# Kernel optimization log

Hardware: AMD Instinct MI355X
Metric: run time of the kernel (lower is better)

## Reference

```python
import jax, jax.numpy as jnp
import numpy as np

B, N_COLS, N_PROMPTS, D = 1024, 256, 128, 256


def _ln(x, g, b, eps=1e-5):
    m = jnp.mean(x, axis=-1, keepdims=True)
    v = jnp.mean(jnp.square(x - m), axis=-1, keepdims=True)
    return (x - m) * jax.lax.rsqrt(v + eps) * g + b


def setup_inputs() -> dict:
    key = jax.random.key(0)
    ks = jax.random.split(key, 10)
    d_rs = D ** -0.5
    return {
        "x": jax.random.normal(ks[0], (B, N_COLS), jnp.float32),
        "prev_cell_out": jax.random.normal(ks[1], (B, N_PROMPTS, D), jnp.float32),
        "feature_emb_weight": jax.random.uniform(ks[2], (N_COLS, D), jnp.float32, -d_rs, d_rs),
        "feature_emb_bias": jax.random.uniform(ks[3], (N_COLS, D), jnp.float32, -d_rs, d_rs),
        "ln_emb_g": jnp.ones((D,), jnp.float32),
        "ln_emb_b": jnp.zeros((D,), jnp.float32),
        "ln_col_g": jnp.ones((D,), jnp.float32),
        "ln_col_b": jnp.zeros((D,), jnp.float32),
        "ln_prompt_g": jnp.ones((D,), jnp.float32),
        "ln_prompt_b": jnp.zeros((D,), jnp.float32),
        # torch Linear(2*D, D): weight [D, 2*D], y = x @ W^T + b
        "dense_imp_w": jax.random.normal(ks[4], (D, 2 * D), jnp.float32) * (2 * D) ** -0.5,
        "dense_imp_b": jnp.zeros((D,), jnp.float32),
        "emb_column": jax.random.normal(ks[5], (N_COLS, D), jnp.float32) * 0.01,
        "emb_prompt": jax.random.normal(ks[6], (N_PROMPTS, D), jnp.float32) * 0.01,
        # dense_expand = Linear(1, n_prompts): weight [n_prompts,1] squeezed -> [n_prompts]
        "expand_w": jax.random.normal(ks[7], (N_PROMPTS,), jnp.float32),
        "expand_b": jax.random.normal(ks[8], (N_PROMPTS,), jnp.float32) * 0.01,
    }


def reference(x, prev_cell_out, feature_emb_weight, feature_emb_bias,
              ln_emb_g, ln_emb_b, ln_col_g, ln_col_b, ln_prompt_g, ln_prompt_b,
              dense_imp_w, dense_imp_b, emb_column, emb_prompt,
              expand_w, expand_b):
    # feature embedding: [B, N, D]
    x_emb = jax.nn.relu(jnp.einsum('bn,nd->bnd', x, feature_emb_weight) + feature_emb_bias)
    x_emb = _ln(x_emb, ln_emb_g, ln_emb_b)
    # prompt update with residual
    xp = jnp.broadcast_to(emb_prompt[None], (x.shape[0], N_PROMPTS, D))  # [B, P, D]
    cat = jnp.concatenate([_ln(xp, ln_prompt_g, ln_prompt_b), prev_cell_out], axis=-1)  # [B, P, 2D]
    xp = jnp.einsum('bpk,dk->bpd', cat, dense_imp_w) + dense_imp_b + xp
    # column keys (shared across batch)
    col = _ln(emb_column, ln_col_g, ln_col_b)  # [N, D]
    mask = jax.nn.softmax(jnp.einsum('bpd,nd->bpn', xp, col), axis=-1)  # [B, P, N]
    V = jnp.einsum('bpn,bnd->bpd', mask, x_emb)  # [B, P, D]
    return V * (1.0 + expand_w)[None, :, None] + expand_b[None, :, None]
```

## Files before the change

kernel.cpp:

```cpp
#include <hip/hip_runtime.h>

#define NCOLS 256
#define NP    128
#define DD    256

typedef _Float16 half2 __attribute__((ext_vector_type(2)));
typedef _Float16 half4 __attribute__((ext_vector_type(4)));
typedef float    f32x4 __attribute__((ext_vector_type(4)));

#define MFMA16(a,b,c) __builtin_amdgcn_mfma_f32_16x16x16f16(a,b,c,0,0,0)

#define WS_COL_LN   0
#define WS_LNP      262144
#define WS_BASE     393216
#define WS_BLOG     524288
#define WS_CW16     655360
#define WS_WB16     786432

#define LDS_CW0   3072
#define LDS_XE0   35840
#define LDS_CW1   68608
#define LDS_XE1   101376
#define SMEM_MAIN 134144


__global__ __launch_bounds__(256) void k0a(
    const float* __restrict__ emb_column, const float* __restrict__ emb_prompt,
    const float* __restrict__ ln_col_g, const float* __restrict__ ln_col_b,
    const float* __restrict__ ln_prompt_g, const float* __restrict__ ln_prompt_b,
    const float* __restrict__ few, const float* __restrict__ feb,
    char* __restrict__ ws)
{
    __shared__ float red[10];
    int blk = blockIdx.x, tid = threadIdx.x;
    if (blk < 384) {
        const float *src, *g, *bb; float* dst;
        if (blk < 256) { int r = blk;     src = emb_column + r*DD; g = ln_col_g;    bb = ln_col_b;    dst = (float*)(ws + WS_COL_LN) + r*DD; }
        else           { int r = blk-256; src = emb_prompt + r*DD; g = ln_prompt_g; bb = ln_prompt_b; dst = (float*)(ws + WS_LNP) + r*DD; }
        float v = src[tid];
        float s = v, q = v*v;
        #pragma unroll
        for (int off = 32; off; off >>= 1) { s += __shfl_xor(s, off); q += __shfl_xor(q, off); }
        int wid = tid >> 6, lane = tid & 63;
        if (lane == 0) { red[wid] = s; red[4+wid] = q; }
        __syncthreads();
        if (tid == 0) {
            float S = red[0]+red[1]+red[2]+red[3];
            float Q = red[4]+red[5]+red[6]+red[7];
            float mu = S * (1.0f/DD);
            float var = Q * (1.0f/DD) - mu*mu;
            red[8] = mu; red[9] = rsqrtf(var + 1e-5f);
        }
        __syncthreads();
        dst[tid] = (v - red[8]) * red[9] * g[tid] + bb[tid];
    } else {
        int base = (blk - 384) * 512;
        half2* wb = (half2*)(ws + WS_WB16);
        #pragma unroll
        for (int j = 0; j < 2; ++j) {
            int idx = base + j*256 + tid;
            half2 h; h[0] = (_Float16)few[idx]; h[1] = (_Float16)feb[idx];
            wb[idx] = h;
        }
    }
}

__global__ __launch_bounds__(256) void k0b(
    const float* __restrict__ diw, const float* __restrict__ dib,
    const float* __restrict__ emb_prompt, char* __restrict__ ws)
{
    __shared__ float rowv[DD];
    int blk = blockIdx.x, tid = threadIdx.x;
    if (blk < 256) {
        int n = blk;
        const float* col_ln = (const float*)(ws + WS_COL_LN);
        rowv[tid] = col_ln[n*DD + tid];
        __syncthreads();
        float acc = 0.f;
        #pragma unroll 4
        for (int d = 0; d < DD; ++d) acc += rowv[d] * diw[d*512 + 256 + tid];
        int nt = n >> 4, lr = n & 15;
        int kc = tid >> 4, lq = (tid >> 2) & 3, j = tid & 3;
        ((_Float16*)(ws + WS_CW16))[((kc*16 + nt)*64 + lq*16 + lr)*4 + j] = (_Float16)acc;
    } else {
        int p = blk - 256;
        const float* lnp = (const float*)(ws + WS_LNP);
        rowv[tid] = lnp[p*DD + tid];
        __syncthreads();
        float acc = 0.f;
        #pragma unroll 4
        for (int k = 0; k < DD; ++k) acc += rowv[k] * diw[tid*512 + k];
        ((float*)(ws + WS_BASE))[p*DD + tid] = acc + dib[tid] + emb_prompt[p*DD + tid];
    }
}

__global__ __launch_bounds__(256) void k0c(char* __restrict__ ws)
{
    __shared__ float bs[DD];
    int p = blockIdx.x, n = threadIdx.x;
    const float* base   = (const float*)(ws + WS_BASE);
    const float* col_ln = (const float*)(ws + WS_COL_LN);
    bs[n] = base[p*DD + n];
    __syncthreads();
    float acc = 0.f;
    #pragma unroll 4
    for (int d = 0; d < DD; ++d) acc += bs[d] * col_ln[n*DD + d];
    ((float*)(ws + WS_BLOG))[p*DD + n] = acc;
}

__global__ __launch_bounds__(512, 2) void trompt_main(
    const float* __restrict__ x, const float* __restrict__ prev,
    const float* __restrict__ expand_w, const float* __restrict__ expand_b,
    const float* __restrict__ ln_emb_g, const float* __restrict__ ln_emb_b,
    const char* __restrict__ ws, float* __restrict__ out)
{
    extern __shared__ char smem[];
    float* x_s  = (float*)(smem);
    float* g_s  = (float*)(smem + 1024);
    float* bb_s = (float*)(smem + 2048);

    const char*  cwbase = ws + WS_CW16;
    const half2* WB     = (const half2*)(ws + WS_WB16);

    int b = blockIdx.x;
    int tid = threadIdx.x;
    int w = tid >> 6, l = tid & 63, lq = l >> 4, lr = l & 15;
    int p = 16*w + lr;

    if (tid < 256) {
        x_s[tid]  = x[b*NCOLS + tid];
        g_s[tid]  = ln_emb_g[tid];
        bb_s[tid] = ln_emb_b[tid];
    }

    half4 pfrag[16];
    {
        const float* prow = prev + ((size_t)b*NP + p)*DD + 4*lq;
        #pragma unroll
        for (int kc = 0; kc < 16; ++kc) {
            f32x4 v = *(const f32x4*)(prow + 16*kc);
            half4 h;
            #pragma unroll
            for (int j = 0; j < 4; ++j) h[j] = (_Float16)v[j];
            pfrag[kc] = h;
        }
    }

    auto stage_cw = [&](int c, char* dstbuf) {
        #pragma unroll
        for (int i = 0; i < 4; ++i) {
            int u = tid + 512*i;
            int kc = u >> 7, rem = u & 127;
            uint4 v = *(const uint4*)(cwbase + kc*8192 + c*2048 + rem*16);
            *(uint4*)(dstbuf + u*16) = v;
        }
    };

    auto compute_xe = [&](int c, char* xebuf) {
        #pragma unroll
        for (int gi = 0; gi < 2; ++gi) {
            int g = w + 8*gi;
            int kc2 = g >> 2, lq2 = g & 3;
            float vj[4][4];
            #pragma unroll
            for (int j = 0; j < 4; ++j) {
                int n = c*64 + 16*kc2 + 4*lq2 + j;
                float xv = x_s[n];
                const half2* wbrow = WB + n*DD;
                float s = 0.f, q = 0.f;
                #pragma unroll
                for (int cc = 0; cc < 4; ++cc) {
                    half2 pp = wbrow[l + 64*cc];
                    float e = fmaf(xv, (float)pp[0], (float)pp[1]);
                    e = e > 0.f ? e : 0.f;
                    vj[j][cc] = e; s += e; q += e*e;
                }
                #pragma unroll
                for (int off = 32; off; off >>= 1) { s += __shfl_xor(s, off); q += __shfl_xor(q, off); }
                float mu = s * (1.0f/DD);
                float rs = rsqrtf(q*(1.0f/DD) - mu*mu + 1e-5f);
                #pragma unroll
                for (int cc = 0; cc < 4; ++cc) {
                    int d = l + 64*cc;
                    vj[j][cc] = (vj[j][cc]-mu)*rs*g_s[d] + bb_s[d];
                }
            }
            #pragma unroll
            for (int cc = 0; cc < 4; ++cc) {
                int dt = 4*cc + (l >> 4);
                half4 h;
                #pragma unroll
                for (int j = 0; j < 4; ++j) h[j] = (_Float16)vj[j][cc];
                *(half4*)(xebuf + (((kc2*16 + dt)*64) + lq2*16 + lr)*8) = h;
            }
        }
    };

    stage_cw(0, smem + LDS_CW0);
    __syncthreads();
    compute_xe(0, smem + LDS_XE0);

    f32x4 acc_v[16];
    #pragma unroll
    for (int dt = 0; dt < 16; ++dt) acc_v[dt] = (f32x4){0.f,0.f,0.f,0.f};
    float m = -1e30f, ll = 0.f;

    const float* blrow = (const float*)(ws + WS_BLOG) + (size_t)p*DD + 4*lq;

    __syncthreads();

    for (int c = 0; c < 4; ++c) {
        char* cwc = smem + ((c & 1) ? LDS_CW1 : LDS_CW0);
        char* xec = smem + ((c & 1) ? LDS_XE1 : LDS_XE0);
        char* cwn = smem + ((c & 1) ? LDS_CW0 : LDS_CW1);
        char* xen = smem + ((c & 1) ? LDS_XE0 : LDS_XE1);

        uint4 st[4];
        if (c < 3) {
            #pragma unroll
            for (int i = 0; i < 4; ++i) {
                int u = tid + 512*i;
                int kc = u >> 7, rem = u & 127;
                st[i] = *(const uint4*)(cwbase + kc*8192 + (c+1)*2048 + rem*16);
            }
        }

        f32x4 acc_c[4];
        #pragma unroll
        for (int nt = 0; nt < 4; ++nt) acc_c[nt] = *(const f32x4*)(blrow + 64*c + 16*nt);
        const char* cwl = cwc + l*8;
        #pragma unroll
        for (int kc = 0; kc < 16; ++kc) {
            const char* fb = cwl + kc*2048;
            half4 a0 = *(const half4*)(fb);
            half4 a1 = *(const half4*)(fb + 512);
            half4 a2 = *(const half4*)(fb + 1024);
            half4 a3 = *(const half4*)(fb + 1536);
            half4 bp = pfrag[kc];
            acc_c[0] = MFMA16(a0, bp, acc_c[0]);
            acc_c[1] = MFMA16(a1, bp, acc_c[1]);
            acc_c[2] = MFMA16(a2, bp, acc_c[2]);
            acc_c[3] = MFMA16(a3, bp, acc_c[3]);
        }

        float pmax = -1e30f;
        #pragma unroll
        for (int nt = 0; nt < 4; ++nt)
            #pragma unroll
            for (int r = 0; r < 4; ++r) pmax = fmaxf(pmax, acc_c[nt][r]);
        pmax = fmaxf(pmax, __shfl_xor(pmax, 16));
        pmax = fmaxf(pmax, __shfl_xor(pmax, 32));
        float mnew = fmaxf(m, pmax);
        float f = __expf(m - mnew);
        m = mnew;
        ll *= f;
        #pragma unroll
        for (int dt = 0; dt < 16; ++dt)
            #pragma unroll
            for (int r = 0; r < 4; ++r) acc_v[dt][r] *= f;

        float csum = 0.f;
        half4 p16c[4];
        #pragma unroll
        for (int nt = 0; nt < 4; ++nt) {
            half4 h;
            #pragma unroll
            for (int r = 0; r < 4; ++r) {
                float e = __expf(acc_c[nt][r] - m);
                csum += e;
                h[r] = (_Float16)e;
            }
            p16c[nt] = h;
        }
        csum += __shfl_xor(csum, 16);
        csum += __shfl_xor(csum, 32);
        ll += csum;

        if (c < 3) {
            compute_xe(c+1, xen);
            #pragma unroll
            for (int i = 0; i < 4; ++i) {
                int u = tid + 512*i;
                *(uint4*)(cwn + u*16) = st[i];
            }
        }

        const char* xel = xec + l*8;
        #pragma unroll
        for (int kc2 = 0; kc2 < 4; ++kc2) {
            half4 bp = p16c[kc2];
            const char* xb = xel + kc2*8192;
            #pragma unroll
            for (int dt = 0; dt < 16; ++dt) {
                half4 a = *(const half4*)(xb + dt*512);
                acc_v[dt] = MFMA16(a, bp, acc_v[dt]);
            }
        }

        __syncthreads();
    }

    {
        float sw = (1.0f + expand_w[p]) / ll;
        float sb = expand_b[p];
        float* orow = out + ((size_t)b*NP + p)*DD + 4*lq;
        #pragma unroll
        for (int dt = 0; dt < 16; ++dt) {
            f32x4 v = acc_v[dt];
            #pragma unroll
            for (int r = 0; r < 4; ++r) v[r] = v[r]*sw + sb;
            *(f32x4*)(orow + 16*dt) = v;
        }
    }
}

extern "C" void kernel_launch(void* const* d_in, const int* in_sizes, int n_in,
                              void* d_out, int out_size, void* d_ws, size_t ws_size,
                              hipStream_t stream) {
    (void)in_sizes; (void)n_in; (void)out_size; (void)ws_size;
    const float* x           = (const float*)d_in[0];
    const float* prev        = (const float*)d_in[1];
    const float* few         = (const float*)d_in[2];
    const float* feb         = (const float*)d_in[3];
    const float* ln_emb_g    = (const float*)d_in[4];
    const float* ln_emb_b    = (const float*)d_in[5];
    const float* ln_col_g    = (const float*)d_in[6];
    const float* ln_col_b    = (const float*)d_in[7];
    const float* ln_prompt_g = (const float*)d_in[8];
    const float* ln_prompt_b = (const float*)d_in[9];
    const float* diw         = (const float*)d_in[10];
    const float* dib         = (const float*)d_in[11];
    const float* emb_column  = (const float*)d_in[12];
    const float* emb_prompt  = (const float*)d_in[13];
    const float* expand_w    = (const float*)d_in[14];
    const float* expand_b    = (const float*)d_in[15];
    char* ws = (char*)d_ws;
    float* out = (float*)d_out;

    k0a<<<512, 256, 0, stream>>>(emb_column, emb_prompt, ln_col_g, ln_col_b,
                                 ln_prompt_g, ln_prompt_b, few, feb, ws);
    k0b<<<384, 256, 0, stream>>>(diw, dib, emb_prompt, ws);
    k0c<<<128, 256, 0, stream>>>(ws);

    (void)hipFuncSetAttribute(reinterpret_cast<const void*>(trompt_main),
                              hipFuncAttributeMaxDynamicSharedMemorySize, SMEM_MAIN);
    trompt_main<<<1024, 512, SMEM_MAIN, stream>>>(x, prev, expand_w, expand_b,
                                                  ln_emb_g, ln_emb_b, ws, out);
}
```

Before: 202.0 us.

## Split fused attention kernel into logit-softmax and PV kernels with fp16 P buffer

Replaces the single flash-style kernel, which used online softmax, with two kernels. The first computes logits and a full softmax per half of the prompts and writes normalized fp16 probabilities into the output buffer as scratch. The second recomputes the embedding tiles and accumulates P·X_emb, then overwrites the output in place. The aim is lower LDS and register pressure per kernel, for higher occupancy and no online rescaling. The cost is an extra global round trip for P and a second launch.

After: 218.9 us. +8.3%, slower.

```diff
diff --git a/kernel.cpp b/kernel.cpp
--- a/kernel.cpp
+++ b/kernel.cpp
@@ -17,11 +17,8 @@
 #define WS_CW16     655360
 #define WS_WB16     786432
 
-#define LDS_CW0   3072
-#define LDS_XE0   35840
-#define LDS_CW1   68608
-#define LDS_XE1   101376
-#define SMEM_MAIN 134144
+#define SMEM_LOGIT 67584
+#define SMEM_PV    34816
 
 
 __global__ __launch_bounds__(256) void k0a(
@@ -108,186 +105,212 @@
     ((float*)(ws + WS_BLOG))[p*DD + n] = acc;
 }
 
-__global__ __launch_bounds__(512, 2) void trompt_main(
-    const float* __restrict__ x, const float* __restrict__ prev,
+__global__ __launch_bounds__(512, 4) void k_logit(
+    const float* __restrict__ prev, const char* __restrict__ ws,
+    char* __restrict__ pbuf)
+{
+    extern __shared__ char smem[];
+    float* sm_m = (float*)(smem + 65536);
+    float* sm_l = (float*)(smem + 66560);
+
+    const char* cwbase = ws + WS_CW16;
+
+    int bid = blockIdx.x;
+    int b = bid >> 1, ph = bid & 1;
+    int tid = threadIdx.x;
+    int w = tid >> 6, l = tid & 63, lq = l >> 4, lr = l & 15;
+    int pt = w >> 1, nh = w & 1;
+    int pl = 16*pt + lr;
+    int p  = 64*ph + pl;
+
+    half4 pfrag[16];
+    {
+        const float* prow = prev + ((size_t)b*NP + p)*DD + 4*lq;
+        #pragma unroll
+        for (int kc = 0; kc < 16; ++kc) {
+            f32x4 v = *(const f32x4*)(prow + 16*kc);
+            half4 h;
+            #pragma unroll
+            for (int j = 0; j < 4; ++j) h[j] = (_Float16)v[j];
+            pfrag[kc] = h;
+        }
+    }
+
+    auto stage_cw = [&](int c, char* dst) {
+        #pragma unroll
+        for (int i = 0; i < 4; ++i) {
+            int u = tid + 512*i;
+            int kc = u >> 7, ntg = (u >> 5) & 3, rem = u & 31;
+            uint4 v = *(const uint4*)(cwbase + kc*8192 + c*2048 + ntg*512 + rem*16);
+            *(uint4*)(dst + u*16) = v;
+        }
+    };
+
+    f32x4 acc[8];
+    {
+        const float* blrow = (const float*)(ws + WS_BLOG) + (size_t)p*DD + 4*lq;
+        #pragma unroll
+        for (int a = 0; a < 8; ++a)
+            acc[a] = *(const f32x4*)(blrow + 16*(4*(a>>1) + 2*nh + (a&1)));
+    }
+
+    stage_cw(0, smem);
+    __syncthreads();
+
+    #pragma unroll
+    for (int c = 0; c < 4; ++c) {
+        char* cwc = smem + ((c & 1) ? 32768 : 0);
+        char* cwn = smem + ((c & 1) ? 0 : 32768);
+
+        uint4 st[4];
+        if (c < 3) {
+            #pragma unroll
+            for (int i = 0; i < 4; ++i) {
+                int u = tid + 512*i;
+                int kc = u >> 7, ntg = (u >> 5) & 3, rem = u & 31;
+                st[i] = *(const uint4*)(cwbase + kc*8192 + (c+1)*2048 + ntg*512 + rem*16);
+            }
+        }
+
+        const char* cwl = cwc + l*8 + nh*1024;
+        #pragma unroll
+        for (int kc = 0; kc < 16; ++kc) {
+            const char* fb = cwl + kc*2048;
+            half4 a0 = *(const half4*)(fb);
+            half4 a1 = *(const half4*)(fb + 512);
+            half4 bp = pfrag[kc];
+            acc[2*c]   = MFMA16(a0, bp, acc[2*c]);
+            acc[2*c+1] = MFMA16(a1, bp, acc[2*c+1]);
+        }
+
+        if (c < 3) {
+            #pragma unroll
+            for (int i = 0; i < 4; ++i) {
+                int u = tid + 512*i;
+                *(uint4*)(cwn + u*16) = st[i];
+            }
+        }
+        __syncthreads();
+    }
+
+    float pmax = -1e30f;
+    #pragma unroll
+    for (int a = 0; a < 8; ++a)
+        #pragma unroll
+        for (int r = 0; r < 4; ++r) pmax = fmaxf(pmax, acc[a][r]);
+    pmax = fmaxf(pmax, __shfl_xor(pmax, 16));
+    pmax = fmaxf(pmax, __shfl_xor(pmax, 32));
+    if (lq == 0) sm_m[nh*64 + pl] = pmax;
+    __syncthreads();
+    float m = fmaxf(pmax, sm_m[(1 ^ nh)*64 + pl]);
+
+    float s = 0.f;
+    #pragma unroll
+    for (int a = 0; a < 8; ++a)
+        #pragma unroll
+        for (int r = 0; r < 4; ++r) { float e = __expf(acc[a][r] - m); acc[a][r] = e; s += e; }
+    s += __shfl_xor(s, 16);
+    s += __shfl_xor(s, 32);
+    if (lq == 0) sm_l[nh*64 + pl] = s;
+    __syncthreads();
+    float inv = 1.0f / (s + sm_l[(1 ^ nh)*64 + pl]);
+
+    char* Pb = pbuf + (size_t)b*131072;
+    #pragma unroll
+    for (int a = 0; a < 8; ++a) {
+        int NT = 4*(a >> 1) + 2*nh + (a & 1);
+        half4 h;
+        #pragma unroll
+        for (int r = 0; r < 4; ++r) h[r] = (_Float16)(acc[a][r] * inv);
+        *(half4*)(Pb + p*512 + NT*32 + lq*8) = h;
+    }
+}
+
+__global__ __launch_bounds__(512, 4) void k_pv(
+    const float* __restrict__ x,
     const float* __restrict__ expand_w, const float* __restrict__ expand_b,
     const float* __restrict__ ln_emb_g, const float* __restrict__ ln_emb_b,
     const char* __restrict__ ws, float* __restrict__ out)
 {
     extern __shared__ char smem[];
-    float* x_s  = (float*)(smem);
-    float* g_s  = (float*)(smem + 1024);
-    float* bb_s = (float*)(smem + 2048);
-
-    const char*  cwbase = ws + WS_CW16;
-    const half2* WB     = (const half2*)(ws + WS_WB16);
+    float* x_s = (float*)smem;
+    char* xe0 = smem + 2048;
+    char* xe1 = smem + 18432;
+
+    const half2* WB = (const half2*)(ws + WS_WB16);
 
     int b = blockIdx.x;
     int tid = threadIdx.x;
     int w = tid >> 6, l = tid & 63, lq = l >> 4, lr = l & 15;
     int p = 16*w + lr;
 
-    if (tid < 256) {
-        x_s[tid]  = x[b*NCOLS + tid];
-        g_s[tid]  = ln_emb_g[tid];
-        bb_s[tid] = ln_emb_b[tid];
-    }
-
-    half4 pfrag[16];
-    {
-        const float* prow = prev + ((size_t)b*NP + p)*DD + 4*lq;
-        #pragma unroll
-        for (int kc = 0; kc < 16; ++kc) {
-            f32x4 v = *(const f32x4*)(prow + 16*kc);
+    if (tid < 256) x_s[tid] = x[b*NCOLS + tid];
+    float gcc[4], bcc[4];
+    #pragma unroll
+    for (int cc = 0; cc < 4; ++cc) {
+        gcc[cc] = ln_emb_g[l + 64*cc];
+        bcc[cc] = ln_emb_b[l + 64*cc];
+    }
+
+    const char* Pb = (const char*)out + (size_t)b*131072;
+
+    auto compute_xe = [&](int c, char* xebuf) {
+        int kc2 = w >> 2, lq2 = w & 3;
+        float vj[4][4];
+        #pragma unroll
+        for (int j = 0; j < 4; ++j) {
+            int n = c*32 + 16*kc2 + 4*lq2 + j;
+            float xv = x_s[n];
+            const half2* wbrow = WB + n*DD;
+            float s = 0.f, q = 0.f;
+            #pragma unroll
+            for (int cc = 0; cc < 4; ++cc) {
+                half2 pp = wbrow[l + 64*cc];
+                float e = fmaf(xv, (float)pp[0], (float)pp[1]);
+                e = e > 0.f ? e : 0.f;
+                vj[j][cc] = e; s += e; q += e*e;
+            }
+            #pragma unroll
+            for (int off = 32; off; off >>= 1) { s += __shfl_xor(s, off); q += __shfl_xor(q, off); }
+            float mu = s * (1.0f/DD);
+            float rs = rsqrtf(q*(1.0f/DD) - mu*mu + 1e-5f);
+            #pragma unroll
+            for (int cc = 0; cc < 4; ++cc)
+                vj[j][cc] = (vj[j][cc]-mu)*rs*gcc[cc] + bcc[cc];
+        }
+        #pragma unroll
+        for (int cc = 0; cc < 4; ++cc) {
+            int dt = 4*cc + (l >> 4);
             half4 h;
             #pragma unroll
-            for (int j = 0; j < 4; ++j) h[j] = (_Float16)v[j];
-            pfrag[kc] = h;
-        }
-    }
-
-    auto stage_cw = [&](int c, char* dstbuf) {
-        #pragma unroll
-        for (int i = 0; i < 4; ++i) {
-            int u = tid + 512*i;
-            int kc = u >> 7, rem = u & 127;
-            uint4 v = *(const uint4*)(cwbase + kc*8192 + c*2048 + rem*16);
-            *(uint4*)(dstbuf + u*16) = v;
+            for (int j = 0; j < 4; ++j) h[j] = (_Float16)vj[j][cc];
+            *(half4*)(xebuf + (((kc2*16 + dt)*64) + lq2*16 + lr)*8) = h;
         }
     };
 
-    auto compute_xe = [&](int c, char* xebuf) {
-        #pragma unroll
-        for (int gi = 0; gi < 2; ++gi) {
-            int g = w + 8*gi;
-            int kc2 = g >> 2, lq2 = g & 3;
-            float vj[4][4];
-            #pragma unroll
-            for (int j = 0; j < 4; ++j) {
-                int n = c*64 + 16*kc2 + 4*lq2 + j;
-                float xv = x_s[n];
-                const half2* wbrow = WB + n*DD;
-                float s = 0.f, q = 0.f;
-                #pragma unroll
-                for (int cc = 0; cc < 4; ++cc) {
-                    half2 pp = wbrow[l + 64*cc];
-                    float e = fmaf(xv, (float)pp[0], (float)pp[1]);
-                    e = e > 0.f ? e : 0.f;
-                    vj[j][cc] = e; s += e; q += e*e;
-                }
-                #pragma unroll
-                for (int off = 32; off; off >>= 1) { s += __shfl_xor(s, off); q += __shfl_xor(q, off); }
-                float mu = s * (1.0f/DD);
-                float rs = rsqrtf(q*(1.0f/DD) - mu*mu + 1e-5f);
-                #pragma unroll
-                for (int cc = 0; cc < 4; ++cc) {
-                    int d = l + 64*cc;
-                    vj[j][cc] = (vj[j][cc]-mu)*rs*g_s[d] + bb_s[d];
-                }
-            }
-            #pragma unroll
-            for (int cc = 0; cc < 4; ++cc) {
-                int dt = 4*cc + (l >> 4);
-                half4 h;
-                #pragma unroll
-                for (int j = 0; j < 4; ++j) h[j] = (_Float16)vj[j][cc];
-                *(half4*)(xebuf + (((kc2*16 + dt)*64) + lq2*16 + lr)*8) = h;
-            }
-        }
-    };
-
-    stage_cw(0, smem + LDS_CW0);
-    __syncthreads();
-    compute_xe(0, smem + LDS_XE0);
+    __syncthreads();
+    compute_xe(0, xe0);
 
     f32x4 acc_v[16];
     #pragma unroll
     for (int dt = 0; dt < 16; ++dt) acc_v[dt] = (f32x4){0.f,0.f,0.f,0.f};
-    float m = -1e30f, ll = 0.f;
-
-    const float* blrow = (const float*)(ws + WS_BLOG) + (size_t)p*DD + 4*lq;
-
-    __syncthreads();
-
-    for (int c = 0; c < 4; ++c) {
-        char* cwc = smem + ((c & 1) ? LDS_CW1 : LDS_CW0);
-        char* xec = smem + ((c & 1) ? LDS_XE1 : LDS_XE0);
-        char* cwn = smem + ((c & 1) ? LDS_CW0 : LDS_CW1);
-        char* xen = smem + ((c & 1) ? LDS_XE0 : LDS_XE1);
-
-        uint4 st[4];
-        if (c < 3) {
-            #pragma unroll
-            for (int i = 0; i < 4; ++i) {
-                int u = tid + 512*i;
-                int kc = u >> 7, rem = u & 127;
-                st[i] = *(const uint4*)(cwbase + kc*8192 + (c+1)*2048 + rem*16);
-            }
-        }
-
-        f32x4 acc_c[4];
-        #pragma unroll
-        for (int nt = 0; nt < 4; ++nt) acc_c[nt] = *(const f32x4*)(blrow + 64*c + 16*nt);
-        const char* cwl = cwc + l*8;
-        #pragma unroll
-        for (int kc = 0; kc < 16; ++kc) {
-            const char* fb = cwl + kc*2048;
-            half4 a0 = *(const half4*)(fb);
-            half4 a1 = *(const half4*)(fb + 512);
-            half4 a2 = *(const half4*)(fb + 1024);
-            half4 a3 = *(const half4*)(fb + 1536);
-            half4 bp = pfrag[kc];
-            acc_c[0] = MFMA16(a0, bp, acc_c[0]);
-            acc_c[1] = MFMA16(a1, bp, acc_c[1]);
-            acc_c[2] = MFMA16(a2, bp, acc_c[2]);
-            acc_c[3] = MFMA16(a3, bp, acc_c[3]);
-        }
-
-        float pmax = -1e30f;
-        #pragma unroll
-        for (int nt = 0; nt < 4; ++nt)
-            #pragma unroll
-            for (int r = 0; r < 4; ++r) pmax = fmaxf(pmax, acc_c[nt][r]);
-        pmax = fmaxf(pmax, __shfl_xor(pmax, 16));
-        pmax = fmaxf(pmax, __shfl_xor(pmax, 32));
-        float mnew = fmaxf(m, pmax);
-        float f = __expf(m - mnew);
-        m = mnew;
-        ll *= f;
-        #pragma unroll
-        for (int dt = 0; dt < 16; ++dt)
-            #pragma unroll
-            for (int r = 0; r < 4; ++r) acc_v[dt][r] *= f;
-
-        float csum = 0.f;
-        half4 p16c[4];
-        #pragma unroll
-        for (int nt = 0; nt < 4; ++nt) {
-            half4 h;
-            #pragma unroll
-            for (int r = 0; r < 4; ++r) {
-                float e = __expf(acc_c[nt][r] - m);
-                csum += e;
-                h[r] = (_Float16)e;
-            }
-            p16c[nt] = h;
-        }
-        csum += __shfl_xor(csum, 16);
-        csum += __shfl_xor(csum, 32);
-        ll += csum;
-
-        if (c < 3) {
-            compute_xe(c+1, xen);
-            #pragma unroll
-            for (int i = 0; i < 4; ++i) {
-                int u = tid + 512*i;
-                *(uint4*)(cwn + u*16) = st[i];
-            }
-        }
+
+    __syncthreads();
+
+    for (int c = 0; c < 8; ++c) {
+        char* xec = (c & 1) ? xe1 : xe0;
+        char* xen = (c & 1) ? xe0 : xe1;
+
+        half4 p16c[2];
+        #pragma unroll
+        for (int kc2 = 0; kc2 < 2; ++kc2)
+            p16c[kc2] = *(const half4*)(Pb + p*512 + c*64 + kc2*32 + lq*8);
+
+        if (c < 7) compute_xe(c+1, xen);
 
         const char* xel = xec + l*8;
         #pragma unroll
-        for (int kc2 = 0; kc2 < 4; ++kc2) {
+        for (int kc2 = 0; kc2 < 2; ++kc2) {
             half4 bp = p16c[kc2];
             const char* xb = xel + kc2*8192;
             #pragma unroll
@@ -301,7 +324,7 @@
     }
 
     {
-        float sw = (1.0f + expand_w[p]) / ll;
+        float sw = 1.0f + expand_w[p];
         float sb = expand_b[p];
         float* orow = out + ((size_t)b*NP + p)*DD + 4*lq;
         #pragma unroll
@@ -342,8 +365,12 @@
     k0b<<<384, 256, 0, stream>>>(diw, dib, emb_prompt, ws);
     k0c<<<128, 256, 0, stream>>>(ws);
 
-    (void)hipFuncSetAttribute(reinterpret_cast<const void*>(trompt_main),
-                              hipFuncAttributeMaxDynamicSharedMemorySize, SMEM_MAIN);
-    trompt_main<<<1024, 512, SMEM_MAIN, stream>>>(x, prev, expand_w, expand_b,
-                                                  ln_emb_g, ln_emb_b, ws, out);
-}
+    (void)hipFuncSetAttribute(reinterpret_cast<const void*>(k_logit),
+                              hipFuncAttributeMaxDynamicSharedMemorySize, SMEM_LOGIT);
+    k_logit<<<2048, 512, SMEM_LOGIT, stream>>>(prev, ws, (char*)d_out);
+
+    (void)hipFuncSetAttribute(reinterpret_cast<const void*>(k_pv),
+                              hipFuncAttributeMaxDynamicSharedMemorySize, SMEM_PV);
+    k_pv<<<1024, 512, SMEM_PV, stream>>>(x, expand_w, expand_b,
+                                         ln_emb_g, ln_emb_b, ws, out);
+}
```
